# Kernel tuning notes

Measured on AMD Instinct MI355X. Metric: run time of the kernel, lower is better.

Reference implementation:

```python
import jax, jax.numpy as jnp
import numpy as np

B, S, E, U = 4, 512, 512, 256

def setup_inputs() -> dict:
    key = jax.random.key(0)
    k1, k2, k3, k4 = jax.random.split(key, 4)
    h1 = jax.random.normal(k1, (B, S, E), dtype=jnp.float32)
    h2 = jax.random.normal(k2, (B, S, E), dtype=jnp.float32)
    # glorot-ish scaled weights
    w = jax.random.normal(k3, (2 * E, U), dtype=jnp.float32) * (2.0 / (2 * E + U)) ** 0.5
    b1 = jnp.zeros((U,), dtype=jnp.float32)
    v = jax.random.normal(k4, (U, 1), dtype=jnp.float32) * (2.0 / (U + 1)) ** 0.5
    b2 = jnp.zeros((1,), dtype=jnp.float32)
    return {"h1": h1, "h2": h2, "w": w, "b1": b1, "v": v, "b2": b2}

def reference(h1, h2, w, b1, v, b2):
    # Original: for each query step i, concat([h1, repeat(h2[:,i])]) @ w.
    # Split w so the concat-matmul becomes two separate projections:
    #   concat([h1_j, h2_i]) @ w == h1_j @ w1 + h2_i @ w2
    E_ = h1.shape[-1]
    w1, w2 = w[:E_], w[E_:]
    key_pre = jnp.einsum('bje,eu->bju', h1, w1)   # [B,Sk,U]
    qry_pre = jnp.einsum('bie,eu->biu', h2, w2)   # [B,Sq,U]
    # energy: [B,Sq,Sk,U]
    t = jnp.tanh(qry_pre[:, :, None, :] + key_pre[:, None, :, :] + b1)
    scores = jnp.einsum('biju,uo->bij', t, v) + b2[0]  # [B,Sq,Sk]
    p = jax.nn.softmax(scores, axis=-1)                # softmax over keys j
    # context per query: sum_j p[b,i,j] * h1[b,j]
    return jnp.einsum('bij,bje->bie', p, h1)           # [B,S,E]
```

## Files before the change

### kernel.cpp

```cpp
#include <hip/hip_runtime.h>
#include <hip/hip_bf16.h>

#define B_ 4
#define S_ 512
#define E_ 512
#define U_ 256

#define KC 2.885390081777927f

#if __has_builtin(__builtin_amdgcn_exp2f)
#define EXP2F(x) __builtin_amdgcn_exp2f(x)
#else
#define EXP2F(x) __exp2f(x)
#endif
#if __has_builtin(__builtin_amdgcn_rcpf)
#define RCPF(x) __builtin_amdgcn_rcpf(x)
#else
#define RCPF(x) (1.0f / (x))
#endif

typedef __attribute__((ext_vector_type(8))) short bf16x8;
typedef __attribute__((ext_vector_type(4))) float f32x4;

__device__ __forceinline__ unsigned short bf16rn(float x) {
    unsigned int u = __float_as_uint(x);
    u = (u + 0x7FFFu + ((u >> 16) & 1u)) >> 16;
    return (unsigned short)u;
}
__device__ __forceinline__ void splitT(float x, short* hi, short* lo) {
    const unsigned u = __float_as_uint(x);
    *hi = (short)(u >> 16);
    const float hf = __uint_as_float(u & 0xFFFF0000u);
    *lo = (short)(__float_as_uint(x - hf) >> 16);
}

__global__ __launch_bounds__(256) void prep_gemm(
    const float* __restrict__ h1, const float* __restrict__ h2,
    const float* __restrict__ w, const float* __restrict__ b1,
    float* __restrict__ ekS, float* __restrict__ eqS)
{
    __shared__ unsigned short WhiL[2][16][64][8];
    __shared__ unsigned short WloL[2][16][64][8];

    const int tid = threadIdx.x;
    const int bid = blockIdx.x;

    const int z = bid >> 8, ngg = (bid >> 5) & 7, mq = bid & 31;

    const int r8 = tid >> 5, ul = tid & 31;
    const int ntc = ul >> 4, l16c = ul & 15;
    const float* __restrict__ Wp = w + (size_t)z * E_ * U_ + ngg * 32 + ul;
#pragma unroll 4
    for (int it = 0; it < 64; ++it) {
        const int k = it * 8 + r8;
        short h, l;
        splitT(Wp[(size_t)k * U_] * KC, &h, &l);
        const int kc = k >> 5, quad = (k >> 3) & 3, jj = k & 7;
        WhiL[ntc][kc][quad * 16 + l16c][jj] = (unsigned short)h;
        WloL[ntc][kc][quad * 16 + l16c][jj] = (unsigned short)l;
    }
    __syncthreads();

    const int wv = tid >> 6, lane = tid & 63;
    const int quad = lane >> 4, l16 = lane & 15;
    const int m0 = (mq * 4 + wv) * 16;
    const float* __restrict__ Arow = (z ? h2 : h1) + (size_t)(m0 + l16) * E_;

    f32x4 acc[2];
    acc[0] = (f32x4){0.f, 0.f, 0.f, 0.f};
    acc[1] = (f32x4){0.f, 0.f, 0.f, 0.f};

    for (int kc = 0; kc < 16; ++kc) {
        const int kb = kc * 32 + quad * 8;
        const float4 x0 = *(const float4*)&Arow[kb];
        const float4 x1 = *(const float4*)&Arow[kb + 4];
        const float xs[8] = {x0.x, x0.y, x0.z, x0.w, x1.x, x1.y, x1.z, x1.w};
        bf16x8 ah, al;
#pragma unroll
        for (int j = 0; j < 8; ++j) {
            short h, l; splitT(xs[j], &h, &l);
            ah[j] = h; al[j] = l;
        }
#pragma unroll
        for (int nt = 0; nt < 2; ++nt) {
            const bf16x8 bh = *(const bf16x8*)&WhiL[nt][kc][lane][0];
            const bf16x8 bl = *(const bf16x8*)&WloL[nt][kc][lane][0];
            acc[nt] = __builtin_amdgcn_mfma_f32_16x16x32_bf16(ah, bh, acc[nt], 0, 0, 0);
            acc[nt] = __builtin_amdgcn_mfma_f32_16x16x32_bf16(ah, bl, acc[nt], 0, 0, 0);
            acc[nt] = __builtin_amdgcn_mfma_f32_16x16x32_bf16(al, bh, acc[nt], 0, 0, 0);
        }
    }

    if (z == 0) {
        const int b = m0 >> 9;
        const int j0 = (m0 & (S_ - 1)) + quad * 4;
#pragma unroll
        for (int nt = 0; nt < 2; ++nt) {
            const int u = (ngg * 2 + nt) * 16 + l16;
            *(float4*)&ekS[((size_t)b * U_ + u) * S_ + j0] =
                make_float4(EXP2F(acc[nt][0]), EXP2F(acc[nt][1]),
                            EXP2F(acc[nt][2]), EXP2F(acc[nt][3]));
        }
    } else {
        const int row = m0 + quad * 4;
#pragma unroll
        for (int nt = 0; nt < 2; ++nt) {
            const int u = (ngg * 2 + nt) * 16 + l16;
            const float bias = KC * b1[u];
#pragma unroll
            for (int r = 0; r < 4; ++r)
                eqS[(size_t)(row + r) * U_ + u] = EXP2F(acc[nt][r] + bias);
        }
    }
}

__device__ __forceinline__ float quadG(float G1, float G2, float G3, float G4,
                                       float4 vq, float acc) {
    const float P12 = G1 * G2, P34 = G3 * G4;
    const float n12 = fmaf(vq.y, G1, vq.x * G2);
    const float n34 = fmaf(vq.w, G3, vq.z * G4);
    const float num = fmaf(n34, P12, n12 * P34);
    return fmaf(num, RCPF(P12 * P34), acc);
}

__global__ __launch_bounds__(512) void scores_kernel(
    const float* __restrict__ ekS, const float* __restrict__ eqS,
    const float* __restrict__ v, unsigned short* __restrict__ Pp,
    const float* __restrict__ h1, bf16x8* __restrict__ h1c)
{
    __shared__ float ssm[8][4];
    const int bid = blockIdx.x;
    const int t = threadIdx.x;

    if (bid >= 512) {
        const int s = (bid - 512) * 512 + t;
        const int lane = s & 63, kc = (s >> 6) & 15, et = (s >> 10) & 31, b = s >> 15;
        const int quad = lane >> 4, l16 = lane & 15;
        const float* __restrict__ src =
            h1 + ((size_t)b * S_ + kc * 32 + quad * 8) * E_ + et * 16 + l16;
        bf16x8 c;
#pragma unroll
        for (int j = 0; j < 8; ++j)
            c[j] = (short)bf16rn(src[(size_t)j * E_]);
        h1c[s] = c;
        return;
    }

    const int b = bid & 3;
    const int i0 = (bid >> 2) * 4;
    const int wv = t >> 6;

    const float4* __restrict__ q0v = (const float4*)(eqS + ((size_t)b * S_ + i0) * U_);
    const float4* __restrict__ q1v = q0v + (U_ / 4);
    const float4* __restrict__ q2v = q0v + 2 * (U_ / 4);
    const float4* __restrict__ q3v = q0v + 3 * (U_ / 4);
    const float4* __restrict__ vv4 = (const float4*)v;
    const float* __restrict__ kb = ekS + (size_t)b * U_ * S_ + t;

    float a0 = 0.f, a1 = 0.f, a2 = 0.f, a3 = 0.f;
#pragma unroll 4
    for (int ub = 0; ub < U_ / 4; ++ub) {
        const float4 vq = vv4[ub];
        const float e0 = kb[(size_t)(ub * 4 + 0) * S_];
        const float e1 = kb[(size_t)(ub * 4 + 1) * S_];
        const float e2 = kb[(size_t)(ub * 4 + 2) * S_];
        const float e3 = kb[(size_t)(ub * 4 + 3) * S_];
        const float4 q0 = q0v[ub], q1 = q1v[ub], q2 = q2v[ub], q3 = q3v[ub];
        a0 = quadG(fmaf(q0.x, e0, 1.f), fmaf(q0.y, e1, 1.f),
                   fmaf(q0.z, e2, 1.f), fmaf(q0.w, e3, 1.f), vq, a0);
        a1 = quadG(fmaf(q1.x, e0, 1.f), fmaf(q1.y, e1, 1.f),
                   fmaf(q1.z, e2, 1.f), fmaf(q1.w, e3, 1.f), vq, a1);
        a2 = quadG(fmaf(q2.x, e0, 1.f), fmaf(q2.y, e1, 1.f),
                   fmaf(q2.z, e2, 1.f), fmaf(q2.w, e3, 1.f), vq, a2);
        a3 = quadG(fmaf(q3.x, e0, 1.f), fmaf(q3.y, e1, 1.f),
                   fmaf(q3.z, e2, 1.f), fmaf(q3.w, e3, 1.f), vq, a3);
    }

    const float p0 = EXP2F(-a0 * KC);
    const float p1 = EXP2F(-a1 * KC);
    const float p2 = EXP2F(-a2 * KC);
    const float p3 = EXP2F(-a3 * KC);
    float s0 = p0, s1 = p1, s2 = p2, s3 = p3;
#pragma unroll
    for (int off = 1; off < 64; off <<= 1) {
        s0 += __shfl_xor(s0, off, 64);
        s1 += __shfl_xor(s1, off, 64);
        s2 += __shfl_xor(s2, off, 64);
        s3 += __shfl_xor(s3, off, 64);
    }
    if ((t & 63) == 0) {
        ssm[wv][0] = s0; ssm[wv][1] = s1; ssm[wv][2] = s2; ssm[wv][3] = s3;
    }
    __syncthreads();
    s0 = ssm[0][0]; s1 = ssm[0][1]; s2 = ssm[0][2]; s3 = ssm[0][3];
#pragma unroll
    for (int k = 1; k < 8; ++k) {
        s0 += ssm[k][0]; s1 += ssm[k][1]; s2 += ssm[k][2]; s3 += ssm[k][3];
    }
    const float r0 = RCPF(s0), r1 = RCPF(s1), r2 = RCPF(s2), r3 = RCPF(s3);

    const int itile = i0 >> 4;
    const int base = (itile * 16 + (t >> 5)) * 64 + (((t >> 3) & 3) << 4);
    unsigned short* __restrict__ pb = Pp + (size_t)b * S_ * S_;
    const int io = i0 & 15, jo = t & 7;
    pb[((base + io + 0) << 3) + jo] = bf16rn(p0 * r0);
    pb[((base + io + 1) << 3) + jo] = bf16rn(p1 * r1);
    pb[((base + io + 2) << 3) + jo] = bf16rn(p2 * r2);
    pb[((base + io + 3) << 3) + jo] = bf16rn(p3 * r3);
}

__global__ __launch_bounds__(256) void pv_gemm(
    const unsigned short* __restrict__ Pp, const bf16x8* __restrict__ h1c,
    float* __restrict__ out)
{
    const int tid = threadIdx.x;
    const int wv = tid >> 6, lane = tid & 63;
    const int quad = lane >> 4, l16 = lane & 15;
    const int wt = blockIdx.x * 4 + wv;
    const int b = wt >> 9, rem = wt & 511;
    const int it = rem >> 4, eg = rem & 15;

    const bf16x8* __restrict__ Ab =
        (const bf16x8*)(Pp + (size_t)b * S_ * S_) + (it * 16) * 64 + lane;
    const bf16x8* __restrict__ Bb =
        h1c + ((b * 32 + eg * 2) * 16) * 64 + lane;

    f32x4 acc[2];
    acc[0] = (f32x4){0.f, 0.f, 0.f, 0.f};
    acc[1] = (f32x4){0.f, 0.f, 0.f, 0.f};

    for (int kc = 0; kc < 16; ++kc) {
        const bf16x8 a8 = Ab[kc * 64];
#pragma unroll
        for (int n = 0; n < 2; ++n) {
            const bf16x8 b8 = Bb[(n * 16 + kc) * 64];
            acc[n] = __builtin_amdgcn_mfma_f32_16x16x32_bf16(a8, b8, acc[n], 0, 0, 0);
        }
    }

    const int i = it * 16 + quad * 4;
#pragma unroll
    for (int n = 0; n < 2; ++n) {
        const int e = (eg * 2 + n) * 16 + l16;
        float* __restrict__ ob = out + ((size_t)b * S_ + i) * E_ + e;
#pragma unroll
        for (int r = 0; r < 4; ++r)
            ob[(size_t)r * E_] = acc[n][r];
    }
}

extern "C" void kernel_launch(void* const* d_in, const int* in_sizes, int n_in,
                              void* d_out, int out_size, void* d_ws, size_t ws_size,
                              hipStream_t stream) {
    const float* h1 = (const float*)d_in[0];
    const float* h2 = (const float*)d_in[1];
    const float* w  = (const float*)d_in[2];
    const float* b1 = (const float*)d_in[3];
    const float* v  = (const float*)d_in[4];
    float* out = (float*)d_out;

    char* ws = (char*)d_ws;
    float* ekS = (float*)ws;                   ws += 2u << 20;
    float* eqS = (float*)ws;                   ws += 2u << 20;
    unsigned short* Pp = (unsigned short*)ws;  ws += 2u << 20;
    bf16x8* h1c = (bf16x8*)ws;

    prep_gemm<<<dim3(512), dim3(256), 0, stream>>>(h1, h2, w, b1, ekS, eqS);
    scores_kernel<<<dim3(768), dim3(512), 0, stream>>>(ekS, eqS, v, Pp, h1, h1c);
    pv_gemm<<<dim3(512), dim3(256), 0, stream>>>(Pp, h1c, out);
}
```

Measured before the change: 115.4 us.

## Pre-split activations to bf16 hi/lo in a separate kernel and interleave key exponentials

Adds a convert kernel that splits h1/h2 into bf16 hi/lo fragments in MFMA order once, with the KC scale moved from the weights to the activations. This avoids redoing the split in every one of the 8 N-group blocks of prep_gemm. The key exponentials are stored in a U-quad-interleaved layout, so scores_kernel reads one float4 per step instead of four strided scalars. The h1 transpose-convert moves out of scores_kernel, which now uses a 2D grid. The cost is an extra kernel launch and extra workspace traffic for the pre-split activations.

```diff
diff --git a/kernel.cpp b/kernel.cpp
--- a/kernel.cpp
+++ b/kernel.cpp
@@ -34,17 +34,55 @@
     *lo = (short)(__float_as_uint(x - hf) >> 16);
 }
 
+__global__ __launch_bounds__(256) void convert_kernel(
+    const float* __restrict__ h1, const float* __restrict__ h2,
+    bf16x8* __restrict__ Af, bf16x8* __restrict__ h1c)
+{
+    const int tid = threadIdx.x;
+    const int bid = blockIdx.x;
+
+    if (bid < 1024) {
+        const int g = bid * 256 + tid;
+        const int lane = g & 63, kc = (g >> 6) & 15, mt = (g >> 10) & 127, z = g >> 17;
+        const int quad = lane >> 4, l16 = lane & 15;
+        const float* __restrict__ src = (z ? h2 : h1)
+            + ((size_t)(mt * 16 + l16)) * E_ + kc * 32 + quad * 8;
+        const float4 x0 = *(const float4*)src;
+        const float4 x1 = *(const float4*)(src + 4);
+        const float xs[8] = {x0.x, x0.y, x0.z, x0.w, x1.x, x1.y, x1.z, x1.w};
+        bf16x8 ah, al;
+#pragma unroll
+        for (int j = 0; j < 8; ++j) {
+            short h, l; splitT(xs[j] * KC, &h, &l);
+            ah[j] = h; al[j] = l;
+        }
+        const size_t o = (((size_t)z * 2 * 128 + mt) * 16 + kc) * 64 + lane;
+        Af[o] = ah;
+        Af[o + (size_t)128 * 16 * 64] = al;
+    } else {
+        const int s = (bid - 1024) * 256 + tid;
+        const int lane = s & 63, kc = (s >> 6) & 15, et = (s >> 10) & 31, b = s >> 15;
+        const int quad = lane >> 4, l16 = lane & 15;
+        const float* __restrict__ src =
+            h1 + ((size_t)b * S_ + kc * 32 + quad * 8) * E_ + et * 16 + l16;
+        bf16x8 c;
+#pragma unroll
+        for (int j = 0; j < 8; ++j)
+            c[j] = (short)bf16rn(src[(size_t)j * E_]);
+        h1c[s] = c;
+    }
+}
+
 __global__ __launch_bounds__(256) void prep_gemm(
-    const float* __restrict__ h1, const float* __restrict__ h2,
+    const bf16x8* __restrict__ Af,
     const float* __restrict__ w, const float* __restrict__ b1,
-    float* __restrict__ ekS, float* __restrict__ eqS)
+    float* __restrict__ ek4, float* __restrict__ eqS)
 {
     __shared__ unsigned short WhiL[2][16][64][8];
     __shared__ unsigned short WloL[2][16][64][8];
 
     const int tid = threadIdx.x;
     const int bid = blockIdx.x;
-
     const int z = bid >> 8, ngg = (bid >> 5) & 7, mq = bid & 31;
 
     const int r8 = tid >> 5, ul = tid & 31;
@@ -54,7 +92,7 @@
     for (int it = 0; it < 64; ++it) {
         const int k = it * 8 + r8;
         short h, l;
-        splitT(Wp[(size_t)k * U_] * KC, &h, &l);
+        splitT(Wp[(size_t)k * U_], &h, &l);
         const int kc = k >> 5, quad = (k >> 3) & 3, jj = k & 7;
         WhiL[ntc][kc][quad * 16 + l16c][jj] = (unsigned short)h;
         WloL[ntc][kc][quad * 16 + l16c][jj] = (unsigned short)l;
@@ -63,24 +101,18 @@
 
     const int wv = tid >> 6, lane = tid & 63;
     const int quad = lane >> 4, l16 = lane & 15;
-    const int m0 = (mq * 4 + wv) * 16;
-    const float* __restrict__ Arow = (z ? h2 : h1) + (size_t)(m0 + l16) * E_;
+    const int mt = mq * 4 + wv, m0 = mt * 16;
+    const bf16x8* __restrict__ Ah =
+        Af + (((size_t)z * 2 * 128 + mt) * 16) * 64 + lane;
+    const bf16x8* __restrict__ Al = Ah + (size_t)128 * 16 * 64;
 
     f32x4 acc[2];
     acc[0] = (f32x4){0.f, 0.f, 0.f, 0.f};
     acc[1] = (f32x4){0.f, 0.f, 0.f, 0.f};
 
     for (int kc = 0; kc < 16; ++kc) {
-        const int kb = kc * 32 + quad * 8;
-        const float4 x0 = *(const float4*)&Arow[kb];
-        const float4 x1 = *(const float4*)&Arow[kb + 4];
-        const float xs[8] = {x0.x, x0.y, x0.z, x0.w, x1.x, x1.y, x1.z, x1.w};
-        bf16x8 ah, al;
-#pragma unroll
-        for (int j = 0; j < 8; ++j) {
-            short h, l; splitT(xs[j], &h, &l);
-            ah[j] = h; al[j] = l;
-        }
+        const bf16x8 ah = Ah[kc * 64];
+        const bf16x8 al = Al[kc * 64];
 #pragma unroll
         for (int nt = 0; nt < 2; ++nt) {
             const bf16x8 bh = *(const bf16x8*)&WhiL[nt][kc][lane][0];
@@ -97,9 +129,11 @@
 #pragma unroll
         for (int nt = 0; nt < 2; ++nt) {
             const int u = (ngg * 2 + nt) * 16 + l16;
-            *(float4*)&ekS[((size_t)b * U_ + u) * S_ + j0] =
-                make_float4(EXP2F(acc[nt][0]), EXP2F(acc[nt][1]),
-                            EXP2F(acc[nt][2]), EXP2F(acc[nt][3]));
+            float* __restrict__ dst =
+                ek4 + ((size_t)b * 64 + (u >> 2)) * 2048 + (u & 3);
+#pragma unroll
+            for (int r = 0; r < 4; ++r)
+                dst[(size_t)(j0 + r) * 4] = EXP2F(acc[nt][r]);
         }
     } else {
         const int row = m0 + quad * 4;
@@ -124,30 +158,13 @@
 }
 
 __global__ __launch_bounds__(512) void scores_kernel(
-    const float* __restrict__ ekS, const float* __restrict__ eqS,
-    const float* __restrict__ v, unsigned short* __restrict__ Pp,
-    const float* __restrict__ h1, bf16x8* __restrict__ h1c)
+    const float* __restrict__ ek4, const float* __restrict__ eqS,
+    const float* __restrict__ v, unsigned short* __restrict__ Pp)
 {
     __shared__ float ssm[8][4];
-    const int bid = blockIdx.x;
+    const int i0 = blockIdx.x * 4;
+    const int b = blockIdx.y;
     const int t = threadIdx.x;
-
-    if (bid >= 512) {
-        const int s = (bid - 512) * 512 + t;
-        const int lane = s & 63, kc = (s >> 6) & 15, et = (s >> 10) & 31, b = s >> 15;
-        const int quad = lane >> 4, l16 = lane & 15;
-        const float* __restrict__ src =
-            h1 + ((size_t)b * S_ + kc * 32 + quad * 8) * E_ + et * 16 + l16;
-        bf16x8 c;
-#pragma unroll
-        for (int j = 0; j < 8; ++j)
-            c[j] = (short)bf16rn(src[(size_t)j * E_]);
-        h1c[s] = c;
-        return;
-    }
-
-    const int b = bid & 3;
-    const int i0 = (bid >> 2) * 4;
     const int wv = t >> 6;
 
     const float4* __restrict__ q0v = (const float4*)(eqS + ((size_t)b * S_ + i0) * U_);
@@ -155,25 +172,22 @@
     const float4* __restrict__ q2v = q0v + 2 * (U_ / 4);
     const float4* __restrict__ q3v = q0v + 3 * (U_ / 4);
     const float4* __restrict__ vv4 = (const float4*)v;
-    const float* __restrict__ kb = ekS + (size_t)b * U_ * S_ + t;
+    const float4* __restrict__ kbb = (const float4*)ek4 + (size_t)b * 64 * 512 + t;
 
     float a0 = 0.f, a1 = 0.f, a2 = 0.f, a3 = 0.f;
 #pragma unroll 4
     for (int ub = 0; ub < U_ / 4; ++ub) {
         const float4 vq = vv4[ub];
-        const float e0 = kb[(size_t)(ub * 4 + 0) * S_];
-        const float e1 = kb[(size_t)(ub * 4 + 1) * S_];
-        const float e2 = kb[(size_t)(ub * 4 + 2) * S_];
-        const float e3 = kb[(size_t)(ub * 4 + 3) * S_];
+        const float4 e = kbb[(size_t)ub * 512];
         const float4 q0 = q0v[ub], q1 = q1v[ub], q2 = q2v[ub], q3 = q3v[ub];
-        a0 = quadG(fmaf(q0.x, e0, 1.f), fmaf(q0.y, e1, 1.f),
-                   fmaf(q0.z, e2, 1.f), fmaf(q0.w, e3, 1.f), vq, a0);
-        a1 = quadG(fmaf(q1.x, e0, 1.f), fmaf(q1.y, e1, 1.f),
-                   fmaf(q1.z, e2, 1.f), fmaf(q1.w, e3, 1.f), vq, a1);
-        a2 = quadG(fmaf(q2.x, e0, 1.f), fmaf(q2.y, e1, 1.f),
-                   fmaf(q2.z, e2, 1.f), fmaf(q2.w, e3, 1.f), vq, a2);
-        a3 = quadG(fmaf(q3.x, e0, 1.f), fmaf(q3.y, e1, 1.f),
-                   fmaf(q3.z, e2, 1.f), fmaf(q3.w, e3, 1.f), vq, a3);
+        a0 = quadG(fmaf(q0.x, e.x, 1.f), fmaf(q0.y, e.y, 1.f),
+                   fmaf(q0.z, e.z, 1.f), fmaf(q0.w, e.w, 1.f), vq, a0);
+        a1 = quadG(fmaf(q1.x, e.x, 1.f), fmaf(q1.y, e.y, 1.f),
+                   fmaf(q1.z, e.z, 1.f), fmaf(q1.w, e.w, 1.f), vq, a1);
+        a2 = quadG(fmaf(q2.x, e.x, 1.f), fmaf(q2.y, e.y, 1.f),
+                   fmaf(q2.z, e.z, 1.f), fmaf(q2.w, e.w, 1.f), vq, a2);
+        a3 = quadG(fmaf(q3.x, e.x, 1.f), fmaf(q3.y, e.y, 1.f),
+                   fmaf(q3.z, e.z, 1.f), fmaf(q3.w, e.w, 1.f), vq, a3);
     }
 
     const float p0 = EXP2F(-a0 * KC);
@@ -260,12 +274,14 @@
     float* out = (float*)d_out;
 
     char* ws = (char*)d_ws;
-    float* ekS = (float*)ws;                   ws += 2u << 20;
+    float* ek4 = (float*)ws;                   ws += 2u << 20;
     float* eqS = (float*)ws;                   ws += 2u << 20;
     unsigned short* Pp = (unsigned short*)ws;  ws += 2u << 20;
-    bf16x8* h1c = (bf16x8*)ws;
-
-    prep_gemm<<<dim3(512), dim3(256), 0, stream>>>(h1, h2, w, b1, ekS, eqS);
-    scores_kernel<<<dim3(768), dim3(512), 0, stream>>>(ekS, eqS, v, Pp, h1, h1c);
+    bf16x8* h1c = (bf16x8*)ws;                 ws += 2u << 20;
+    bf16x8* Af  = (bf16x8*)ws;
+
+    convert_kernel<<<dim3(1536), dim3(256), 0, stream>>>(h1, h2, Af, h1c);
+    prep_gemm<<<dim3(512), dim3(256), 0, stream>>>(Af, w, b1, ek4, eqS);
+    scores_kernel<<<dim3(S_ / 4, B_), dim3(512), 0, stream>>>(ek4, eqS, v, Pp);
     pv_gemm<<<dim3(512), dim3(256), 0, stream>>>(Pp, h1c, out);
 }
```

Measured after the change: 114.6 us. No clear change (-0.7%).
